# Performance work log

Measured on AMD Instinct MI355X. Metric: run time of the kernel, lower is better.

## Reference

```python
import jax, jax.numpy as jnp
import numpy as np

D_MODEL = 1024
N_HEADS = 16
D_HEAD = D_MODEL // N_HEADS


def setup_inputs() -> dict:
    key = jax.random.key(0)
    ks = jax.random.split(key, 5)
    B, T = 2, 2048
    x = jax.random.normal(ks[0], (B, T, D_MODEL), dtype=jnp.float32)
    s = 1.0 / np.sqrt(D_MODEL)
    W_qkv = jax.random.normal(ks[1], (D_MODEL, 3 * D_MODEL), dtype=jnp.float32) * s
    b_qkv = jnp.zeros((3 * D_MODEL,), dtype=jnp.float32)
    W_proj = jax.random.normal(ks[2], (D_MODEL, D_MODEL), dtype=jnp.float32) * s
    b_proj = jnp.zeros((D_MODEL,), dtype=jnp.float32)
    return {"x": x, "W_qkv": W_qkv, "b_qkv": b_qkv, "W_proj": W_proj, "b_proj": b_proj}


def reference(x, W_qkv, b_qkv, W_proj, b_proj):
    B, T, C = x.shape
    qkv = x @ W_qkv + b_qkv                      # [B,T,3C]
    q, k, v = jnp.split(qkv, 3, axis=-1)
    # [B,T,C] -> [B,H,T,Dh]
    def to_heads(t):
        return t.reshape(B, T, N_HEADS, D_HEAD).transpose(0, 2, 1, 3)
    q, k, v = to_heads(q), to_heads(k), to_heads(v)
    scale = 1.0 / np.sqrt(D_HEAD).astype(np.float32)
    scores = jnp.einsum('bhqd,bhkd->bhqk', q, k) * scale  # [B,H,T,T]
    causal = jnp.tril(jnp.ones((T, T), dtype=bool))
    scores = jnp.where(causal, scores, -jnp.inf)
    attn = jax.nn.softmax(scores, axis=-1)
    out = jnp.einsum('bhqk,bhkd->bhqd', attn, v)          # [B,H,T,Dh]
    out = out.transpose(0, 2, 1, 3).reshape(B, T, C)
    return out @ W_proj + b_proj
```

## Files before the change

### kernel.cpp

```cpp
#include <hip/hip_runtime.h>
#include <hip/hip_bf16.h>
#include <cstdint>


using u16 = unsigned short;
using u32 = unsigned int;

typedef __bf16 bf16x8 __attribute__((ext_vector_type(8)));
typedef float f32x4 __attribute__((ext_vector_type(4)));

#define AS1 __attribute__((address_space(1)))
#define AS3 __attribute__((address_space(3)))

__device__ __forceinline__ u16 f2bf(float f) {
  u32 u = __float_as_uint(f);
  u += 0x7fffu + ((u >> 16) & 1u);
  return (u16)(u >> 16);
}
__device__ __forceinline__ u32 cvtpk(float a, float b) {
  u32 r;
  asm("v_cvt_pk_bf16_f32 %0, %1, %2" : "=v"(r) : "v"(a), "v"(b));
  return r;
}

__global__ __launch_bounds__(256) void prep(const float* __restrict__ x,
                                            u16* __restrict__ xb,
                                            const float* __restrict__ W0,
                                            u16* __restrict__ T0,
                                            const float* __restrict__ W1,
                                            u16* __restrict__ T1) {
  const int bx = blockIdx.x;
  const int tid = threadIdx.x;
  if (bx < 4096) {
    const int i = bx * 256 + tid;
    float4 v = ((const float4*)x)[i];
    ushort4 o;
    o.x = f2bf(v.x); o.y = f2bf(v.y); o.z = f2bf(v.z); o.w = f2bf(v.w);
    ((ushort4*)xb)[i] = o;
    return;
  }
  __shared__ float t[32][33];
  const int idx = bx - 4096;
  const int bxx = idx & 127, by = idx >> 7;
  const float* W; u16* Wt; int N, n0;
  if (bxx < 96) { W = W0; Wt = T0; N = 3072; n0 = bxx * 32; }
  else          { W = W1; Wt = T1; N = 1024; n0 = (bxx - 96) * 32; }
  const int k0 = by * 32;
  const int tx = tid & 31, ty = tid >> 5;
#pragma unroll
  for (int i = 0; i < 4; ++i)
    t[ty + i * 8][tx] = W[(size_t)(k0 + ty + i * 8) * N + n0 + tx];
  __syncthreads();
#pragma unroll
  for (int i = 0; i < 4; ++i)
    Wt[(size_t)(n0 + ty + i * 8) * 1024 + k0 + tx] = f2bf(t[tx][ty + i * 8]);
}

#define MFMA16 __builtin_amdgcn_mfma_f32_16x16x32_bf16

__global__ __launch_bounds__(512, 2) void gemm_qkv(const u16* __restrict__ A,
                                                   const u16* __restrict__ Bt,
                                                   const float* __restrict__ bias,
                                                   u16* __restrict__ qb,
                                                   u16* __restrict__ KF,
                                                   u16* __restrict__ VF,
                                                   float sc_val) {
  constexpr int NT = 16;
  constexpr int BUFO = 7 * 4096;
  __shared__ __align__(16) u16 sm[2 * BUFO];

  const int tid  = threadIdx.x;
  const int lane = tid & 63;
  const int w    = tid >> 6;
  const int quad = lane >> 4;
  const int l15  = lane & 15;

  const int bid = blockIdx.x;
  const int xcd = bid & 7, c = bid >> 3;
  const int mt = (xcd >> 1) * 4 + (c & 3);
  const int nt = (xcd & 1) * 8 + (c >> 2);
  const int bm = mt * 256, bn = nt * 192;

  const int wr = (w >> 2) * 128;
  const int wc = (w & 3) * 48;

  const int srow = tid >> 3;
  const int scol = (((tid & 7) ^ ((tid >> 3) & 7)) << 3);

#define STAGEA(ch, ktile, bufo)                                                 \
  __builtin_amdgcn_global_load_lds(                                             \
      (AS1 const void*)(A + (size_t)(bm + (ch) * 64 + srow) * 1024 +            \
                        ((ktile) << 6) + scol),                                 \
      (AS3 void*)(sm + (bufo) + (ch) * 4096 + tid * 8), 16, 0, 0)
#define STAGEB(ch, ktile, bufo)                                                 \
  __builtin_amdgcn_global_load_lds(                                             \
      (AS1 const void*)(Bt + (size_t)(bn + (ch) * 64 + srow) * 1024 +           \
                        ((ktile) << 6) + scol),                                 \
      (AS3 void*)(sm + (bufo) + (4 + (ch)) * 4096 + tid * 8), 16, 0, 0)

  const int ca = (w >> 2) * 2;
  int abase_lo[4], abase_hi[4], bbase[3];
#pragma unroll
  for (int mi = 0; mi < 4; ++mi) {
    abase_lo[mi] = (ca + 0) * 4096 + (mi * 16 + l15) * 64;
    abase_hi[mi] = (ca + 1) * 4096 + (mi * 16 + l15) * 64;
  }
#pragma unroll
  for (int ni = 0; ni < 3; ++ni) {
    const int rb = wc + ni * 16 + l15;
    bbase[ni] = (4 + (rb >> 6)) * 4096 + (rb & 63) * 64;
  }
  const int sw0 = ((quad ^ (l15 & 7)) << 3);
  const int sw1 = sw0 ^ 32;

  STAGEA(0, 0, 0); STAGEA(1, 0, 0); STAGEA(2, 0, 0); STAGEA(3, 0, 0);
  STAGEB(0, 0, 0); STAGEB(1, 0, 0); STAGEB(2, 0, 0);
  STAGEB(0, 1, BUFO); STAGEB(1, 1, BUFO);
  STAGEB(2, 1, BUFO); STAGEA(0, 1, BUFO); STAGEA(1, 1, BUFO);
  asm volatile("s_waitcnt vmcnt(5)" ::: "memory");
  __builtin_amdgcn_s_barrier();

  f32x4 acc[8][3] = {};
  bf16x8 alo[4][2], ahi[4][2], b[3][2];

#pragma unroll 2
  for (int j = 0; j < NT; ++j) {
    const int bo  = (j & 1) * BUFO;
    const int nbo = bo ^ BUFO;
    const u16* smb = sm + bo;

#pragma unroll
    for (int mi = 0; mi < 4; ++mi) {
      alo[mi][0] = *(const bf16x8*)(smb + abase_lo[mi] + sw0);
      alo[mi][1] = *(const bf16x8*)(smb + abase_lo[mi] + sw1);
    }
#pragma unroll
    for (int ni = 0; ni < 2; ++ni) {
      b[ni][0] = *(const bf16x8*)(smb + bbase[ni] + sw0);
      b[ni][1] = *(const bf16x8*)(smb + bbase[ni] + sw1);
    }
    if (j + 1 < NT) { STAGEA(2, j + 1, nbo); STAGEA(3, j + 1, nbo); }
    __builtin_amdgcn_s_barrier();
    asm volatile("s_waitcnt lgkmcnt(0)" ::: "memory");
    __builtin_amdgcn_s_setprio(1);
#pragma unroll
    for (int mi = 0; mi < 4; ++mi)
#pragma unroll
      for (int ni = 0; ni < 2; ++ni) {
        acc[mi][ni] = MFMA16(alo[mi][0], b[ni][0], acc[mi][ni], 0, 0, 0);
        acc[mi][ni] = MFMA16(alo[mi][1], b[ni][1], acc[mi][ni], 0, 0, 0);
      }
    __builtin_amdgcn_s_setprio(0);
    __builtin_amdgcn_s_barrier();

#pragma unroll
    for (int mi = 0; mi < 4; ++mi) {
      ahi[mi][0] = *(const bf16x8*)(smb + abase_hi[mi] + sw0);
      ahi[mi][1] = *(const bf16x8*)(smb + abase_hi[mi] + sw1);
    }
    b[2][0] = *(const bf16x8*)(smb + bbase[2] + sw0);
    b[2][1] = *(const bf16x8*)(smb + bbase[2] + sw1);
    if (j + 2 < NT) { STAGEB(0, j + 2, bo); STAGEB(1, j + 2, bo); }
    __builtin_amdgcn_s_barrier();
    asm volatile("s_waitcnt lgkmcnt(0)" ::: "memory");
    __builtin_amdgcn_s_setprio(1);
#pragma unroll
    for (int mi = 0; mi < 4; ++mi) {
      acc[mi][2] = MFMA16(alo[mi][0], b[2][0], acc[mi][2], 0, 0, 0);
      acc[mi][2] = MFMA16(alo[mi][1], b[2][1], acc[mi][2], 0, 0, 0);
      acc[4 + mi][0] = MFMA16(ahi[mi][0], b[0][0], acc[4 + mi][0], 0, 0, 0);
      acc[4 + mi][0] = MFMA16(ahi[mi][1], b[0][1], acc[4 + mi][0], 0, 0, 0);
    }
    __builtin_amdgcn_s_setprio(0);
    __builtin_amdgcn_s_barrier();

    if (j + 2 < NT) { STAGEB(2, j + 2, bo); STAGEA(0, j + 2, bo); STAGEA(1, j + 2, bo); }
    __builtin_amdgcn_s_barrier();
    __builtin_amdgcn_s_setprio(1);
#pragma unroll
    for (int mi = 0; mi < 4; ++mi)
#pragma unroll
      for (int ni = 1; ni < 3; ++ni) {
        acc[4 + mi][ni] = MFMA16(ahi[mi][0], b[ni][0], acc[4 + mi][ni], 0, 0, 0);
        acc[4 + mi][ni] = MFMA16(ahi[mi][1], b[ni][1], acc[4 + mi][ni], 0, 0, 0);
      }
    __builtin_amdgcn_s_setprio(0);
    if (j + 2 < NT)
      asm volatile("s_waitcnt vmcnt(5)" ::: "memory");
    else
      asm volatile("s_waitcnt vmcnt(0)" ::: "memory");
    __builtin_amdgcn_s_barrier();
  }
#undef STAGEA
#undef STAGEB

  const int crow0 = bm + wr + (quad << 2);
  const int ccol0 = bn + wc + l15;
#pragma unroll
  for (int ni = 0; ni < 3; ++ni) {
    const int n = ccol0 + ni * 16;
    const float bv = bias[n];
    if (n < 1024) {
#pragma unroll
      for (int mi = 0; mi < 8; ++mi) {
        const int m0 = crow0 + mi * 16;
#pragma unroll
        for (int r = 0; r < 4; ++r)
          qb[(size_t)(m0 + r) * 1024 + n] = f2bf((acc[mi][ni][r] + bv) * sc_val);
      }
    } else if (n < 2048) {
      const int hk = (n - 1024) >> 6;
      const int d  = (n - 1024) & 63;
      const int hh = d >> 5, qd = (d >> 3) & 3, jj = d & 7;
#pragma unroll
      for (int mi = 0; mi < 8; ++mi) {
#pragma unroll
        for (int r = 0; r < 4; ++r) {
          const int t  = crow0 + mi * 16 + r;
          const int bb = t >> 11, tt = t & 2047;
          const int kt = tt >> 6, mm = (tt >> 4) & 3, l = tt & 15;
          KF[((size_t)((bb * 16 + hk) * 32 + kt) * 8 + mm * 2 + hh) * 512 +
             (qd * 16 + l) * 8 + jj] = f2bf(acc[mi][ni][r] + bv);
        }
      }
    } else {
      const int hv = (n - 2048) >> 6;
      const int d  = (n - 2048) & 63;
      const int di = d >> 4, l = d & 15;
#pragma unroll
      for (int mi = 0; mi < 8; ++mi) {
#pragma unroll
        for (int r = 0; r < 4; ++r) {
          const int t  = crow0 + mi * 16 + r;
          const int bb = t >> 11, tt = t & 2047;
          const int kt = tt >> 6, to = tt & 63;
          const int mq = to >> 4, qd2 = (to >> 2) & 3, rr = to & 3;
          const int hh = mq >> 1, jj = (mq & 1) * 4 + rr;
          VF[((size_t)((bb * 16 + hv) * 32 + kt) * 8 + hh * 4 + di) * 512 +
             (qd2 * 16 + l) * 8 + jj] = f2bf(acc[mi][ni][r] + bv);
        }
      }
    }
  }
}

__global__ __launch_bounds__(256) void gemm_proj(const u16* __restrict__ A,
                                                 const u16* __restrict__ Bt,
                                                 const float* __restrict__ bias,
                                                 float* __restrict__ C) {
  constexpr int BM = 128, BN = 64, BK = 32;
  constexpr int K = 1024, N = 1024;
  __shared__ __align__(16) u16 lA[BM * BK];
  __shared__ __align__(16) u16 lB[BN * BK];
  const int tid  = threadIdx.x;
  const int lane = tid & 63;
  const int wave = tid >> 6;
  const int bm = blockIdx.x * BM;
  const int bn = blockIdx.y * BN;
  const int wr = wave * 32;

  f32x4 acc[2][4] = {};

  const int f0 = (wave << 10) + (lane << 4);
  const int f1 = f0 + 4096;
  const int ar0 = f0 >> 6, ac0 = (f0 & 63) >> 1;
  const int ar1 = f1 >> 6, ac1 = (f1 & 63) >> 1;

  const int arow = wr + (lane & 15);
  const int brow = (lane & 15);
  const int kk   = (lane >> 4) << 3;

  for (int k0 = 0; k0 < K; k0 += BK) {
    __builtin_amdgcn_global_load_lds((AS1 const void*)(A + (size_t)(bm + ar0) * K + k0 + ac0),
                                     (AS3 void*)(lA + (wave << 9)), 16, 0, 0);
    __builtin_amdgcn_global_load_lds((AS1 const void*)(A + (size_t)(bm + ar1) * K + k0 + ac1),
                                     (AS3 void*)(lA + ((wave + 4) << 9)), 16, 0, 0);
    __builtin_amdgcn_global_load_lds((AS1 const void*)(Bt + (size_t)(bn + ar0) * K + k0 + ac0),
                                     (AS3 void*)(lB + (wave << 9)), 16, 0, 0);
    __syncthreads();

    bf16x8 af[2], bfr[4];
#pragma unroll
    for (int mi = 0; mi < 2; ++mi)
      af[mi] = *(const bf16x8*)&lA[(arow + mi * 16) * BK + kk];
#pragma unroll
    for (int ni = 0; ni < 4; ++ni)
      bfr[ni] = *(const bf16x8*)&lB[(brow + ni * 16) * BK + kk];
#pragma unroll
    for (int mi = 0; mi < 2; ++mi)
#pragma unroll
      for (int ni = 0; ni < 4; ++ni)
        acc[mi][ni] = __builtin_amdgcn_mfma_f32_16x16x32_bf16(af[mi], bfr[ni],
                                                              acc[mi][ni], 0, 0, 0);
    __syncthreads();
  }

  const int crow0 = bm + wr + ((lane >> 4) << 2);
  const int ccol0 = bn + (lane & 15);
#pragma unroll
  for (int ni = 0; ni < 4; ++ni) {
    const int n = ccol0 + ni * 16;
    const float bv = bias[n];
#pragma unroll
    for (int mi = 0; mi < 2; ++mi) {
      const int m0 = crow0 + mi * 16;
#pragma unroll
      for (int r = 0; r < 4; ++r)
        C[(size_t)(m0 + r) * N + n] = acc[mi][ni][r] + bv;
    }
  }
}

__global__ __launch_bounds__(128) void attn_bal(const u16* __restrict__ qb,
                                                const u16* __restrict__ KF,
                                                const u16* __restrict__ VF,
                                                u16* __restrict__ out) {
  const int bid = blockIdx.x;
  const int g32 = 63 - ((bid >> 3) & 63);
  const int bh  = (bid & 7) | ((bid >> 9) << 3);
  const int b = bh >> 4, h = bh & 15;
  const int tid = threadIdx.x;
  const int lane = tid & 63;
  const int par  = tid >> 6;
  const int quad = lane >> 4;
  const int l15  = lane & 15;
  const int q0 = g32 * 32;
  const int ktmax = g32 >> 1;

  __shared__ float CB[64][41];

  const u16* qbase = qb + (size_t)b * 2048 * 1024 + h * 64;
  bf16x8 qf[2][2];
#pragma unroll
  for (int g = 0; g < 2; ++g)
#pragma unroll
    for (int hh = 0; hh < 2; ++hh)
      qf[g][hh] = *(const bf16x8*)(qbase + (size_t)(q0 + g * 16 + l15) * 1024 +
                                   hh * 32 + quad * 8);

  const size_t fb = (size_t)bh * 32 * 4096 + lane * 8;
  const u16* kfb = KF + fb;
  const u16* vfb = VF + fb;

  f32x4 accO[2][4] = {};
  f32x4 accL[2] = {};

  union { u32 u4[4]; bf16x8 v; } onesu;
  onesu.u4[0] = onesu.u4[1] = onesu.u4[2] = onesu.u4[3] = 0x3f803f80u;
  const bf16x8 onesf = onesu.v;

  bf16x8 kA[4][2], kB[4][2];
  {
    const u16* kp = kfb + (size_t)par * 4096;
#pragma unroll
    for (int m = 0; m < 4; ++m)
#pragma unroll
      for (int hh = 0; hh < 2; ++hh)
        kA[m][hh] = *(const bf16x8*)(kp + (m * 2 + hh) * 512);
  }

  auto tile = [&](int kt, bf16x8 (&KC)[4][2], bf16x8 (&KN)[4][2]) {
    const u16* vp = vfb + (size_t)kt * 4096;
    bf16x8 vfr[2][4];
#pragma unroll
    for (int hh = 0; hh < 2; ++hh)
#pragma unroll
      for (int di = 0; di < 4; ++di)
        vfr[hh][di] = *(const bf16x8*)(vp + (hh * 4 + di) * 512);
    const int ktn = (kt + 2 <= ktmax) ? kt + 2 : ktmax;
    const u16* kpn = kfb + (size_t)ktn * 4096;
#pragma unroll
    for (int m = 0; m < 4; ++m)
#pragma unroll
      for (int hh = 0; hh < 2; ++hh)
        KN[m][hh] = *(const bf16x8*)(kpn + (m * 2 + hh) * 512);

    const bool diag = (kt == ktmax);
    bf16x8 ap[2][2];
#pragma unroll
    for (int g = 0; g < 2; ++g) {
      f32x4 sT[4] = {};
#pragma unroll
      for (int m = 0; m < 4; ++m) {
        sT[m] = MFMA16(KC[m][0], qf[g][0], sT[m], 0, 0, 0);
        sT[m] = MFMA16(KC[m][1], qf[g][1], sT[m], 0, 0, 0);
      }
      float pv[4][4];
      if (diag) {
        const int qgl = q0 + g * 16 + l15;
#pragma unroll
        for (int m = 0; m < 4; ++m)
#pragma unroll
          for (int r = 0; r < 4; ++r) {
            const bool msk = (kt * 64 + m * 16 + quad * 4 + r) > qgl;
            pv[m][r] = msk ? 0.f : __builtin_amdgcn_exp2f(sT[m][r]);
          }
      } else {
#pragma unroll
        for (int m = 0; m < 4; ++m)
#pragma unroll
          for (int r = 0; r < 4; ++r)
            pv[m][r] = __builtin_amdgcn_exp2f(sT[m][r]);
      }
      union { u32 u4[4]; bf16x8 v; } t0, t1;
      t0.u4[0] = cvtpk(pv[0][0], pv[0][1]);
      t0.u4[1] = cvtpk(pv[0][2], pv[0][3]);
      t0.u4[2] = cvtpk(pv[1][0], pv[1][1]);
      t0.u4[3] = cvtpk(pv[1][2], pv[1][3]);
      t1.u4[0] = cvtpk(pv[2][0], pv[2][1]);
      t1.u4[1] = cvtpk(pv[2][2], pv[2][3]);
      t1.u4[2] = cvtpk(pv[3][0], pv[3][1]);
      t1.u4[3] = cvtpk(pv[3][2], pv[3][3]);
      ap[g][0] = t0.v;
      ap[g][1] = t1.v;
    }

#pragma unroll
    for (int hh = 0; hh < 2; ++hh)
#pragma unroll
      for (int di = 0; di < 4; ++di) {
        bf16x8 bv = vfr[hh][di];
#pragma unroll
        for (int g = 0; g < 2; ++g)
          accO[g][di] = MFMA16(ap[g][hh], bv, accO[g][di], 0, 0, 0);
      }
#pragma unroll
    for (int g = 0; g < 2; ++g) {
      accL[g] = MFMA16(ap[g][0], onesf, accL[g], 0, 0, 0);
      accL[g] = MFMA16(ap[g][1], onesf, accL[g], 0, 0, 0);
    }
  };

  for (int kt = par; kt <= ktmax; ) {
    tile(kt, kA, kB); kt += 2;
    if (kt > ktmax) break;
    tile(kt, kB, kA); kt += 2;
  }

  if (par) {
    float* cb = CB[lane];
#pragma unroll
    for (int g = 0; g < 2; ++g) {
#pragma unroll
      for (int di = 0; di < 4; ++di)
#pragma unroll
        for (int r = 0; r < 4; ++r)
          cb[g * 16 + di * 4 + r] = accO[g][di][r];
#pragma unroll
      for (int r = 0; r < 4; ++r)
        cb[32 + g * 4 + r] = accL[g][r];
    }
  }
  __syncthreads();
  if (!par) {
    const float* cb = CB[lane];
#pragma unroll
    for (int g = 0; g < 2; ++g) {
#pragma unroll
      for (int di = 0; di < 4; ++di)
#pragma unroll
        for (int r = 0; r < 4; ++r)
          accO[g][di][r] += cb[g * 16 + di * 4 + r];
#pragma unroll
      for (int r = 0; r < 4; ++r)
        accL[g][r] += cb[32 + g * 4 + r];
    }

#pragma unroll
    for (int g = 0; g < 2; ++g)
#pragma unroll
      for (int r = 0; r < 4; ++r) {
        const float inv = 1.f / accL[g][r];
        const int q = q0 + g * 16 + quad * 4 + r;
        u16* op = out + (size_t)(b * 2048 + q) * 1024 + h * 64 + l15;
#pragma unroll
        for (int di = 0; di < 4; ++di)
          op[di * 16] = f2bf(accO[g][di][r] * inv);
      }
  }
}

extern "C" void kernel_launch(void* const* d_in, const int* in_sizes, int n_in,
                              void* d_out, int out_size, void* d_ws, size_t ws_size,
                              hipStream_t stream) {
  const float* x     = (const float*)d_in[0];
  const float* Wqkv  = (const float*)d_in[1];
  const float* bqkv  = (const float*)d_in[2];
  const float* Wproj = (const float*)d_in[3];
  const float* bproj = (const float*)d_in[4];
  float* out = (float*)d_out;

  char* ws = (char*)d_ws;
  u16* xb     = (u16*)(ws);
  u16* wqkvT  = (u16*)(ws + 8388608);
  u16* wprojT = (u16*)(ws + 14680064);
  u16* qb     = (u16*)(ws + 16777216);
  u16* KF     = (u16*)(ws + 25165824);
  u16* VF     = (u16*)(ws + 33554432);
  u16* att    = (u16*)(ws + 41943040);

  constexpr float cs = 0.18033688011f;

  prep<<<8192, 256, 0, stream>>>(x, xb, Wqkv, wqkvT, Wproj, wprojT);

  gemm_qkv<<<dim3(256), 512, 0, stream>>>(xb, wqkvT, bqkv, qb, KF, VF, cs);

  attn_bal<<<dim3(2048), 128, 0, stream>>>(qb, KF, VF, att);

  gemm_proj<<<dim3(32, 16), 256, 0, stream>>>(att, wprojT, bproj, out);
}
```

Before: 168.3 us.

## Pair causal query groups per block and double-buffer V loads in attention

Each attention block now processes two 32-row query groups, a long one (63-u) and a short one (u), so every block does roughly equal causal work, and the grid is halved. V fragments are now double-buffered and prefetched alongside K for the next tile instead of being loaded at the start of each tile. Launch bounds request two blocks per CU. The aim is to cut tail imbalance and load latency, in exchange for higher register pressure and an extra barrier between the two groups.

Result: faster. 159.3 us (-5.3%).

```diff
diff --git a/kernel.cpp b/kernel.cpp
--- a/kernel.cpp
+++ b/kernel.cpp
@@ -311,173 +311,188 @@
   }
 }
 
-__global__ __launch_bounds__(128) void attn_bal(const u16* __restrict__ qb,
-                                                const u16* __restrict__ KF,
-                                                const u16* __restrict__ VF,
-                                                u16* __restrict__ out) {
+__global__ __launch_bounds__(128, 2) void attn_bal(const u16* __restrict__ qb,
+                                                   const u16* __restrict__ KF,
+                                                   const u16* __restrict__ VF,
+                                                   u16* __restrict__ out) {
   const int bid = blockIdx.x;
-  const int g32 = 63 - ((bid >> 3) & 63);
-  const int bh  = (bid & 7) | ((bid >> 9) << 3);
+  const int c   = bid >> 3;
+  const int u   = c & 31;
+  const int bh  = (bid & 7) | ((c >> 5) << 3);
   const int b = bh >> 4, h = bh & 15;
   const int tid = threadIdx.x;
   const int lane = tid & 63;
   const int par  = tid >> 6;
   const int quad = lane >> 4;
   const int l15  = lane & 15;
-  const int q0 = g32 * 32;
-  const int ktmax = g32 >> 1;
 
   __shared__ float CB[64][41];
 
   const u16* qbase = qb + (size_t)b * 2048 * 1024 + h * 64;
-  bf16x8 qf[2][2];
-#pragma unroll
-  for (int g = 0; g < 2; ++g)
-#pragma unroll
-    for (int hh = 0; hh < 2; ++hh)
-      qf[g][hh] = *(const bf16x8*)(qbase + (size_t)(q0 + g * 16 + l15) * 1024 +
-                                   hh * 32 + quad * 8);
-
   const size_t fb = (size_t)bh * 32 * 4096 + lane * 8;
   const u16* kfb = KF + fb;
   const u16* vfb = VF + fb;
 
-  f32x4 accO[2][4] = {};
-  f32x4 accL[2] = {};
-
   union { u32 u4[4]; bf16x8 v; } onesu;
   onesu.u4[0] = onesu.u4[1] = onesu.u4[2] = onesu.u4[3] = 0x3f803f80u;
   const bf16x8 onesf = onesu.v;
 
-  bf16x8 kA[4][2], kB[4][2];
-  {
-    const u16* kp = kfb + (size_t)par * 4096;
-#pragma unroll
-    for (int m = 0; m < 4; ++m)
+  u16* const outb = out + (size_t)b * 2048 * 1024 + h * 64 + l15;
+
+  auto run_group = [&](int g32) {
+    const int q0 = g32 * 32;
+    const int ktmax = g32 >> 1;
+
+    bf16x8 qf[2][2];
+#pragma unroll
+    for (int g = 0; g < 2; ++g)
 #pragma unroll
       for (int hh = 0; hh < 2; ++hh)
-        kA[m][hh] = *(const bf16x8*)(kp + (m * 2 + hh) * 512);
-  }
-
-  auto tile = [&](int kt, bf16x8 (&KC)[4][2], bf16x8 (&KN)[4][2]) {
-    const u16* vp = vfb + (size_t)kt * 4096;
-    bf16x8 vfr[2][4];
-#pragma unroll
-    for (int hh = 0; hh < 2; ++hh)
-#pragma unroll
-      for (int di = 0; di < 4; ++di)
-        vfr[hh][di] = *(const bf16x8*)(vp + (hh * 4 + di) * 512);
-    const int ktn = (kt + 2 <= ktmax) ? kt + 2 : ktmax;
-    const u16* kpn = kfb + (size_t)ktn * 4096;
-#pragma unroll
-    for (int m = 0; m < 4; ++m)
+        qf[g][hh] = *(const bf16x8*)(qbase + (size_t)(q0 + g * 16 + l15) * 1024 +
+                                     hh * 32 + quad * 8);
+
+    f32x4 accO[2][4] = {};
+    f32x4 accL[2] = {};
+
+    bf16x8 kA[4][2], kB[4][2], vA[2][4], vB[2][4];
+    {
+      const u16* kp = kfb + (size_t)par * 4096;
+      const u16* vp = vfb + (size_t)par * 4096;
+#pragma unroll
+      for (int m = 0; m < 4; ++m)
+#pragma unroll
+        for (int hh = 0; hh < 2; ++hh)
+          kA[m][hh] = *(const bf16x8*)(kp + (m * 2 + hh) * 512);
 #pragma unroll
       for (int hh = 0; hh < 2; ++hh)
-        KN[m][hh] = *(const bf16x8*)(kpn + (m * 2 + hh) * 512);
-
-    const bool diag = (kt == ktmax);
-    bf16x8 ap[2][2];
-#pragma unroll
-    for (int g = 0; g < 2; ++g) {
-      f32x4 sT[4] = {};
-#pragma unroll
-      for (int m = 0; m < 4; ++m) {
-        sT[m] = MFMA16(KC[m][0], qf[g][0], sT[m], 0, 0, 0);
-        sT[m] = MFMA16(KC[m][1], qf[g][1], sT[m], 0, 0, 0);
-      }
-      float pv[4][4];
-      if (diag) {
-        const int qgl = q0 + g * 16 + l15;
-#pragma unroll
-        for (int m = 0; m < 4; ++m)
-#pragma unroll
-          for (int r = 0; r < 4; ++r) {
-            const bool msk = (kt * 64 + m * 16 + quad * 4 + r) > qgl;
-            pv[m][r] = msk ? 0.f : __builtin_amdgcn_exp2f(sT[m][r]);
-          }
-      } else {
-#pragma unroll
-        for (int m = 0; m < 4; ++m)
+#pragma unroll
+        for (int di = 0; di < 4; ++di)
+          vA[hh][di] = *(const bf16x8*)(vp + (hh * 4 + di) * 512);
+    }
+
+    auto tile = [&](int kt, bf16x8 (&KC)[4][2], bf16x8 (&KN)[4][2],
+                    bf16x8 (&VC)[2][4], bf16x8 (&VN)[2][4]) {
+      const int ktn = (kt + 2 <= ktmax) ? kt + 2 : ktmax;
+      const u16* kpn = kfb + (size_t)ktn * 4096;
+      const u16* vpn = vfb + (size_t)ktn * 4096;
+#pragma unroll
+      for (int m = 0; m < 4; ++m)
+#pragma unroll
+        for (int hh = 0; hh < 2; ++hh)
+          KN[m][hh] = *(const bf16x8*)(kpn + (m * 2 + hh) * 512);
+#pragma unroll
+      for (int hh = 0; hh < 2; ++hh)
+#pragma unroll
+        for (int di = 0; di < 4; ++di)
+          VN[hh][di] = *(const bf16x8*)(vpn + (hh * 4 + di) * 512);
+
+      const bool diag = (kt == ktmax);
+      bf16x8 ap[2][2];
+#pragma unroll
+      for (int g = 0; g < 2; ++g) {
+        f32x4 sT[4] = {};
+#pragma unroll
+        for (int m = 0; m < 4; ++m) {
+          sT[m] = MFMA16(KC[m][0], qf[g][0], sT[m], 0, 0, 0);
+          sT[m] = MFMA16(KC[m][1], qf[g][1], sT[m], 0, 0, 0);
+        }
+        float pv[4][4];
+        if (diag) {
+          const int qgl = q0 + g * 16 + l15;
+#pragma unroll
+          for (int m = 0; m < 4; ++m)
+#pragma unroll
+            for (int r = 0; r < 4; ++r) {
+              const bool msk = (kt * 64 + m * 16 + quad * 4 + r) > qgl;
+              pv[m][r] = msk ? 0.f : __builtin_amdgcn_exp2f(sT[m][r]);
+            }
+        } else {
+#pragma unroll
+          for (int m = 0; m < 4; ++m)
+#pragma unroll
+            for (int r = 0; r < 4; ++r)
+              pv[m][r] = __builtin_amdgcn_exp2f(sT[m][r]);
+        }
+        union { u32 u4[4]; bf16x8 v; } t0, t1;
+        t0.u4[0] = cvtpk(pv[0][0], pv[0][1]);
+        t0.u4[1] = cvtpk(pv[0][2], pv[0][3]);
+        t0.u4[2] = cvtpk(pv[1][0], pv[1][1]);
+        t0.u4[3] = cvtpk(pv[1][2], pv[1][3]);
+        t1.u4[0] = cvtpk(pv[2][0], pv[2][1]);
+        t1.u4[1] = cvtpk(pv[2][2], pv[2][3]);
+        t1.u4[2] = cvtpk(pv[3][0], pv[3][1]);
+        t1.u4[3] = cvtpk(pv[3][2], pv[3][3]);
+        ap[g][0] = t0.v;
+        ap[g][1] = t1.v;
+      }
+
+#pragma unroll
+      for (int hh = 0; hh < 2; ++hh)
+#pragma unroll
+        for (int di = 0; di < 4; ++di) {
+          bf16x8 bv = VC[hh][di];
+#pragma unroll
+          for (int g = 0; g < 2; ++g)
+            accO[g][di] = MFMA16(ap[g][hh], bv, accO[g][di], 0, 0, 0);
+        }
+#pragma unroll
+      for (int g = 0; g < 2; ++g) {
+        accL[g] = MFMA16(ap[g][0], onesf, accL[g], 0, 0, 0);
+        accL[g] = MFMA16(ap[g][1], onesf, accL[g], 0, 0, 0);
+      }
+    };
+
+    for (int kt = par; kt <= ktmax; ) {
+      tile(kt, kA, kB, vA, vB); kt += 2;
+      if (kt > ktmax) break;
+      tile(kt, kB, kA, vB, vA); kt += 2;
+    }
+
+    if (par) {
+      float* cb = CB[lane];
+#pragma unroll
+      for (int g = 0; g < 2; ++g) {
+#pragma unroll
+        for (int di = 0; di < 4; ++di)
 #pragma unroll
           for (int r = 0; r < 4; ++r)
-            pv[m][r] = __builtin_amdgcn_exp2f(sT[m][r]);
-      }
-      union { u32 u4[4]; bf16x8 v; } t0, t1;
-      t0.u4[0] = cvtpk(pv[0][0], pv[0][1]);
-      t0.u4[1] = cvtpk(pv[0][2], pv[0][3]);
-      t0.u4[2] = cvtpk(pv[1][0], pv[1][1]);
-      t0.u4[3] = cvtpk(pv[1][2], pv[1][3]);
-      t1.u4[0] = cvtpk(pv[2][0], pv[2][1]);
-      t1.u4[1] = cvtpk(pv[2][2], pv[2][3]);
-      t1.u4[2] = cvtpk(pv[3][0], pv[3][1]);
-      t1.u4[3] = cvtpk(pv[3][2], pv[3][3]);
-      ap[g][0] = t0.v;
-      ap[g][1] = t1.v;
-    }
-
-#pragma unroll
-    for (int hh = 0; hh < 2; ++hh)
-#pragma unroll
-      for (int di = 0; di < 4; ++di) {
-        bf16x8 bv = vfr[hh][di];
-#pragma unroll
-        for (int g = 0; g < 2; ++g)
-          accO[g][di] = MFMA16(ap[g][hh], bv, accO[g][di], 0, 0, 0);
-      }
-#pragma unroll
-    for (int g = 0; g < 2; ++g) {
-      accL[g] = MFMA16(ap[g][0], onesf, accL[g], 0, 0, 0);
-      accL[g] = MFMA16(ap[g][1], onesf, accL[g], 0, 0, 0);
-    }
+            cb[g * 16 + di * 4 + r] = accO[g][di][r];
+#pragma unroll
+        for (int r = 0; r < 4; ++r)
+          cb[32 + g * 4 + r] = accL[g][r];
+      }
+    }
+    __syncthreads();
+    if (!par) {
+      const float* cb = CB[lane];
+#pragma unroll
+      for (int g = 0; g < 2; ++g) {
+#pragma unroll
+        for (int di = 0; di < 4; ++di)
+#pragma unroll
+          for (int r = 0; r < 4; ++r)
+            accO[g][di][r] += cb[g * 16 + di * 4 + r];
+#pragma unroll
+        for (int r = 0; r < 4; ++r)
+          accL[g][r] += cb[32 + g * 4 + r];
+      }
+#pragma unroll
+      for (int g = 0; g < 2; ++g)
+#pragma unroll
+        for (int r = 0; r < 4; ++r) {
+          const float inv = 1.f / accL[g][r];
+          const int q = q0 + g * 16 + quad * 4 + r;
+          u16* op = outb + (size_t)q * 1024;
+#pragma unroll
+          for (int di = 0; di < 4; ++di)
+            op[di * 16] = f2bf(accO[g][di][r] * inv);
+        }
+    }
+    __syncthreads();
   };
 
-  for (int kt = par; kt <= ktmax; ) {
-    tile(kt, kA, kB); kt += 2;
-    if (kt > ktmax) break;
-    tile(kt, kB, kA); kt += 2;
-  }
-
-  if (par) {
-    float* cb = CB[lane];
-#pragma unroll
-    for (int g = 0; g < 2; ++g) {
-#pragma unroll
-      for (int di = 0; di < 4; ++di)
-#pragma unroll
-        for (int r = 0; r < 4; ++r)
-          cb[g * 16 + di * 4 + r] = accO[g][di][r];
-#pragma unroll
-      for (int r = 0; r < 4; ++r)
-        cb[32 + g * 4 + r] = accL[g][r];
-    }
-  }
-  __syncthreads();
-  if (!par) {
-    const float* cb = CB[lane];
-#pragma unroll
-    for (int g = 0; g < 2; ++g) {
-#pragma unroll
-      for (int di = 0; di < 4; ++di)
-#pragma unroll
-        for (int r = 0; r < 4; ++r)
-          accO[g][di][r] += cb[g * 16 + di * 4 + r];
-#pragma unroll
-      for (int r = 0; r < 4; ++r)
-        accL[g][r] += cb[32 + g * 4 + r];
-    }
-
-#pragma unroll
-    for (int g = 0; g < 2; ++g)
-#pragma unroll
-      for (int r = 0; r < 4; ++r) {
-        const float inv = 1.f / accL[g][r];
-        const int q = q0 + g * 16 + quad * 4 + r;
-        u16* op = out + (size_t)(b * 2048 + q) * 1024 + h * 64 + l15;
-#pragma unroll
-        for (int di = 0; di < 4; ++di)
-          op[di * 16] = f2bf(accO[g][di][r] * inv);
-      }
-  }
+  run_group(63 - u);
+  run_group(u);
 }
 
 extern "C" void kernel_launch(void* const* d_in, const int* in_sizes, int n_in,
@@ -505,7 +520,7 @@
 
   gemm_qkv<<<dim3(256), 512, 0, stream>>>(xb, wqkvT, bqkv, qb, KF, VF, cs);
 
-  attn_bal<<<dim3(2048), 128, 0, stream>>>(qb, KF, VF, att);
+  attn_bal<<<dim3(1024), 128, 0, stream>>>(qb, KF, VF, att);
 
   gemm_proj<<<dim3(32, 16), 256, 0, stream>>>(att, wprojT, bproj, out);
 }
```
